# Kernel tuning notes

Measured on AMD Instinct MI355X. Metric: run time of the kernel, lower is better.

## Reference

```python
import jax, jax.numpy as jnp
import numpy as np

B, N, T_TOK, FEAT, H = 32, 64, 512, 768, 256


def setup_inputs() -> dict:
    key = jax.random.key(0)
    ks = jax.random.split(key, 16)
    p = lambda k, s: jax.random.normal(k, s, jnp.float32) * 0.02
    return {
        "hidden_state": jax.random.normal(ks[0], (B, T_TOK, FEAT), jnp.float32),
        "W_red": p(ks[1], (FEAT, H)), "b_red": jnp.zeros((H,), jnp.float32),
        "W_cat": p(ks[2], (2 * H, H)), "b_cat": jnp.zeros((H,), jnp.float32),
        "W_x": p(ks[3], (H, 3 * H)), "Us_zr": p(ks[4], (H, 2 * H)),
        "Us_h": p(ks[5], (H, H)), "b_g": jnp.zeros((3 * H,), jnp.float32),
        "W_e": p(ks[6], (H, 2)), "b_e": jnp.zeros((2,), jnp.float32),
        "W_c": p(ks[7], (H, 2)), "b_c": jnp.zeros((2,), jnp.float32),
        "W_t": p(ks[8], (H, 2)), "b_t": jnp.zeros((2,), jnp.float32),
        "bert_clause_b": jnp.sort(jax.random.randint(ks[9], (B, N), 0, T_TOK), axis=1),
        "y_mask_b": jnp.ones((B, N), jnp.int32),
    }


def _mdrnn(X, mask2d, W_x, Us_zr, Us_h, b_g):
    # Masked 2D GRU scanning the [B,N,N,H] doc matrix from top-left.
    Bh, Nn, Hd = X.shape[0], X.shape[1], Us_h.shape[0]
    xg = X @ W_x + b_g                       # precomputed input gates [B,N,N,3H]
    mf = mask2d.astype(X.dtype)[..., None]   # [B,N,N,1]

    def col_step(s_left, cols):
        xg_ij, s_up, m_ij = cols             # [B,3H], [B,H], [B,1]
        s_prev = 0.5 * (s_left + s_up)       # fuse left + up states
        zr = jax.nn.sigmoid(xg_ij[:, :2 * Hd] + s_prev @ Us_zr)
        z, r = zr[:, :Hd], zr[:, Hd:]
        h = jnp.tanh(xg_ij[:, 2 * Hd:] + (r * s_prev) @ Us_h)
        s = ((1.0 - z) * s_prev + z * h) * m_ij
        return s, s

    def row_step(prev_row, ins):
        xg_row, m_row = ins                  # [N,B,3H], [N,B,1]
        init = jnp.zeros((Bh, Hd), X.dtype)
        _, row = jax.lax.scan(col_step, init, (xg_row, jnp.swapaxes(prev_row, 0, 1), m_row))
        row = jnp.swapaxes(row, 0, 1)        # [B,N,H]
        return row, row

    xg_t = jnp.transpose(xg, (1, 2, 0, 3))   # [N(i), N(j), B, 3H]
    mf_t = jnp.transpose(mf, (1, 2, 0, 3))
    init_row = jnp.zeros((Bh, Nn, Hd), X.dtype)
    _, rows = jax.lax.scan(row_step, init_row, (xg_t, mf_t))
    return jnp.transpose(rows, (1, 0, 2, 3))  # [B,N,N,H]


def reference(hidden_state, W_red, b_red, W_cat, b_cat, W_x, Us_zr, Us_h, b_g,
              W_e, b_e, W_c, b_c, W_t, b_t, bert_clause_b, y_mask_b):
    # batched_index_select: gather clause-start token states
    doc = jnp.take_along_axis(hidden_state, bert_clause_b[..., None], axis=1)  # [B,N,FEAT]
    r = doc @ W_red + b_red                                                    # [B,N,H]
    Bh, Nn, Hd = r.shape
    # CatReduce: pairwise concat(r_i, r_j) -> Linear; then ReLU
    xi = jnp.broadcast_to(r[:, :, None, :], (Bh, Nn, Nn, Hd))
    xj = jnp.broadcast_to(r[:, None, :, :], (Bh, Nn, Nn, Hd))
    X = jax.nn.relu(jnp.concatenate([xi, xj], axis=-1) @ W_cat + b_cat)        # [B,N,N,H]
    mask2d = y_mask_b[:, None, :] & y_mask_b[:, :, None]                       # [B,N,N]
    Tm = _mdrnn(X, mask2d, W_x, Us_zr, Us_h, b_g)                              # [B,N,N,H]
    diag = jnp.transpose(jnp.diagonal(Tm, axis1=1, axis2=2), (0, 2, 1))        # [B,N,H]
    pred_e = diag @ W_e + b_e
    pred_c = diag @ W_c + b_c
    couples_pred = Tm @ W_t + b_t
    return couples_pred, pred_e, pred_c
```

## Files before the change

kernel.cpp:

```cpp
#include <hip/hip_runtime.h>
#include <hip/hip_bf16.h>

typedef float f32x4 __attribute__((ext_vector_type(4)));
typedef __bf16 bf16x8 __attribute__((ext_vector_type(8)));

using as1c_t = __attribute__((address_space(1))) const char;
using as3_t  = __attribute__((address_space(3))) char;

static __device__ __forceinline__ float sigmoidf_(float x) {
  return 1.f / (1.f + __expf(-x));
}
static __device__ __forceinline__ __bf16 bfc(float x) { return (__bf16)x; }

__global__ __launch_bounds__(256) void k_r(const float* __restrict__ hidden,
    const float* __restrict__ Wred, const float* __restrict__ bred,
    const int* __restrict__ cidx, float* __restrict__ r) {
  __shared__ float docsT[768][8];
  const int bx = blockIdx.x;
  const int b = bx >> 3, n0 = (bx & 7) * 8;
  const int t = threadIdx.x;
  #pragma unroll
  for (int g = 0; g < 8; ++g) {
    const int tok = cidx[b * 64 + n0 + g];
    const float* src = hidden + ((size_t)b * 512 + tok) * 768;
    for (int f = t; f < 768; f += 256) docsT[f][g] = src[f];
  }
  __syncthreads();
  float acc[8];
  #pragma unroll
  for (int g = 0; g < 8; ++g) acc[g] = bred[t];
  for (int f = 0; f < 768; ++f) {
    const float w = Wred[f * 256 + t];
    const float4 d0 = *(const float4*)&docsT[f][0];
    const float4 d1 = *(const float4*)&docsT[f][4];
    acc[0] = fmaf(d0.x, w, acc[0]); acc[1] = fmaf(d0.y, w, acc[1]);
    acc[2] = fmaf(d0.z, w, acc[2]); acc[3] = fmaf(d0.w, w, acc[3]);
    acc[4] = fmaf(d1.x, w, acc[4]); acc[5] = fmaf(d1.y, w, acc[5]);
    acc[6] = fmaf(d1.z, w, acc[6]); acc[7] = fmaf(d1.w, w, acc[7]);
  }
  #pragma unroll
  for (int g = 0; g < 8; ++g) r[((size_t)(b * 64 + n0 + g)) * 256 + t] = acc[g];
}

__global__ __launch_bounds__(256) void k_ab(const float* __restrict__ r,
    const float* __restrict__ Wcat, const float* __restrict__ bcat,
    float* __restrict__ Ai, float* __restrict__ Aj) {
  __shared__ float rT[256][8];
  const int bx = blockIdx.x;
  const int b = bx >> 3, n0 = (bx & 7) * 8;
  const int t = threadIdx.x;
  #pragma unroll
  for (int g = 0; g < 8; ++g)
    rT[t][g] = r[((size_t)(b * 64 + n0 + g)) * 256 + t];
  __syncthreads();
  float ai[8], aj[8];
  #pragma unroll
  for (int g = 0; g < 8; ++g) { ai[g] = bcat[t]; aj[g] = 0.f; }
  for (int k = 0; k < 256; ++k) {
    const float w0 = Wcat[k * 256 + t];
    const float w1 = Wcat[(256 + k) * 256 + t];
    const float4 d0 = *(const float4*)&rT[k][0];
    const float4 d1 = *(const float4*)&rT[k][4];
    ai[0] = fmaf(d0.x, w0, ai[0]); aj[0] = fmaf(d0.x, w1, aj[0]);
    ai[1] = fmaf(d0.y, w0, ai[1]); aj[1] = fmaf(d0.y, w1, aj[1]);
    ai[2] = fmaf(d0.z, w0, ai[2]); aj[2] = fmaf(d0.z, w1, aj[2]);
    ai[3] = fmaf(d0.w, w0, ai[3]); aj[3] = fmaf(d0.w, w1, aj[3]);
    ai[4] = fmaf(d1.x, w0, ai[4]); aj[4] = fmaf(d1.x, w1, aj[4]);
    ai[5] = fmaf(d1.y, w0, ai[5]); aj[5] = fmaf(d1.y, w1, aj[5]);
    ai[6] = fmaf(d1.z, w0, ai[6]); aj[6] = fmaf(d1.z, w1, aj[6]);
    ai[7] = fmaf(d1.w, w0, ai[7]); aj[7] = fmaf(d1.w, w1, aj[7]);
  }
  #pragma unroll
  for (int g = 0; g < 8; ++g) {
    Ai[((size_t)(b * 64 + n0 + g)) * 256 + t] = ai[g];
    Aj[((size_t)(b * 64 + n0 + g)) * 256 + t] = aj[g];
  }
}

__global__ __launch_bounds__(256) void k_wt(const float* __restrict__ Wx,
                                            __hip_bfloat16* __restrict__ WxT) {
  const int n = blockIdx.x, k = threadIdx.x;
  WxT[n * 256 + k] = __float2bfloat16(Wx[k * 768 + n]);
}

__global__ __launch_bounds__(256) void k_gemm(const float* __restrict__ Ai,
    const float* __restrict__ Aj, const __hip_bfloat16* __restrict__ WxT,
    const float* __restrict__ bg, __hip_bfloat16* __restrict__ xg,
    const int b_off) {
  __shared__ alignas(128) char smem[32768];
  char* const smA = smem;
  char* const smB = smem + 16384;
  const int t = threadIdx.x;
  const int lane = t & 63, w = t >> 6;
  const int wr = w >> 1, wc = w & 1;
  const int m0 = blockIdx.x * 128;
  const int n0 = blockIdx.y * 128;
  const char* const Wb = (const char*)WxT;

  const int b = b_off + (m0 >> 12);
  const int ibase = (m0 >> 6) & 63;
  const int rr = t >> 1, half = t & 1;
  const int jj_ = rr & 63, ii_ = ibase + (rr >> 6);
  const float* const aiRow = Ai + ((size_t)b * 64 + ii_) * 256 + half * 32;
  const float* const ajRow = Aj + ((size_t)b * 64 + jj_) * 256 + half * 32;
  char* const dstA = smA + rr * 128 + half * 64;

  f32x4 acc[4][4];
  const f32x4 zero = {0.f, 0.f, 0.f, 0.f};
  #pragma unroll
  for (int a2 = 0; a2 < 4; ++a2)
    #pragma unroll
    for (int b2 = 0; b2 < 4; ++b2) acc[a2][b2] = zero;

  for (int s = 0; s < 4; ++s) {
    const int k0 = s * 64;
    #pragma unroll
    for (int q = 0; q < 4; ++q) {
      const float4 a0 = *(const float4*)(aiRow + k0 + q * 8);
      const float4 a1 = *(const float4*)(aiRow + k0 + q * 8 + 4);
      const float4 c0 = *(const float4*)(ajRow + k0 + q * 8);
      const float4 c1 = *(const float4*)(ajRow + k0 + q * 8 + 4);
      bf16x8 v;
      v[0] = bfc(fmaxf(a0.x + c0.x, 0.f)); v[1] = bfc(fmaxf(a0.y + c0.y, 0.f));
      v[2] = bfc(fmaxf(a0.z + c0.z, 0.f)); v[3] = bfc(fmaxf(a0.w + c0.w, 0.f));
      v[4] = bfc(fmaxf(a1.x + c1.x, 0.f)); v[5] = bfc(fmaxf(a1.y + c1.y, 0.f));
      v[6] = bfc(fmaxf(a1.z + c1.z, 0.f)); v[7] = bfc(fmaxf(a1.w + c1.w, 0.f));
      *(bf16x8*)(dstA + q * 16) = v;
    }
    #pragma unroll
    for (int q = 0; q < 4; ++q) {
      const int chunk = w * 4 + q;
      const int tt2 = chunk * 1024 + lane * 16;
      const int row = tt2 >> 7;
      const int kb = tt2 & 0x7f;
      __builtin_amdgcn_global_load_lds(
          (as1c_t*)(Wb + (size_t)(n0 + row) * 512 + s * 128 + kb),
          (as3_t*)(smB + chunk * 1024), 16, 0, 0);
    }
    __syncthreads();
    #pragma unroll
    for (int kk = 0; kk < 2; ++kk) {
      bf16x8 af[4], bfr[4];
      const int kloc = kk * 64 + ((lane >> 4) << 4);
      #pragma unroll
      for (int ft = 0; ft < 4; ++ft) {
        const int rowa = wr * 64 + ft * 16 + (lane & 15);
        af[ft] = *(const bf16x8*)(smA + rowa * 128 + kloc);
      }
      #pragma unroll
      for (int fn = 0; fn < 4; ++fn) {
        const int rowb = wc * 64 + fn * 16 + (lane & 15);
        bfr[fn] = *(const bf16x8*)(smB + rowb * 128 + kloc);
      }
      #pragma unroll
      for (int ft = 0; ft < 4; ++ft)
        #pragma unroll
        for (int fn = 0; fn < 4; ++fn)
          acc[ft][fn] = __builtin_amdgcn_mfma_f32_16x16x32_bf16(
              af[ft], bfr[fn], acc[ft][fn], 0, 0, 0);
    }
    __syncthreads();
  }

  #pragma unroll
  for (int ft = 0; ft < 4; ++ft) {
    const int mbase = m0 + wr * 64 + ft * 16 + ((lane >> 4) << 2);
    #pragma unroll
    for (int fn = 0; fn < 4; ++fn) {
      const int n = n0 + wc * 64 + fn * 16 + (lane & 15);
      const float bias = bg[n];
      #pragma unroll
      for (int jj = 0; jj < 4; ++jj)
        xg[(size_t)(mbase + jj) * 768 + n] = __float2bfloat16(acc[ft][fn][jj] + bias);
    }
  }
}

__global__ __launch_bounds__(256) void k_diag(const int d, const int ilo,
    const int b_off, const __hip_bfloat16* __restrict__ xg,
    const float* __restrict__ Uzr, const float* __restrict__ Ush,
    const float* __restrict__ Sr, float* __restrict__ Sw,
    const float* __restrict__ Wt, const float* __restrict__ bt,
    const int* __restrict__ ym,
    float* __restrict__ couples, float* __restrict__ diagbuf) {
  __shared__ float sp[256][8];
  __shared__ float rs[256][8];
  __shared__ float red[4][16];
  const int t = threadIdx.x;
  const int i = ilo + blockIdx.x;
  const int j = d - i;
  const int b0 = b_off + blockIdx.y * 8;

  #pragma unroll
  for (int bb = 0; bb < 8; ++bb) {
    const int b = b0 + bb;
    const size_t base = ((size_t)(b * 64 + i)) * 256 + t;
    const float sl = (j > 0) ? Sr[base] : 0.f;
    const float su = (i > 0) ? Sr[base - 256] : 0.f;
    sp[t][bb] = 0.5f * (sl + su);
  }
  __syncthreads();

  const int c = t;
  float accz[8], accr[8];
  #pragma unroll
  for (int bb = 0; bb < 8; ++bb) {
    const size_t xrow = ((size_t)(b0 + bb - b_off) * 4096 + (size_t)i * 64 + j) * 768;
    accz[bb] = __bfloat162float(xg[xrow + c]);
    accr[bb] = __bfloat162float(xg[xrow + 256 + c]);
  }
  for (int k = 0; k < 256; ++k) {
    const float w0 = Uzr[k * 512 + c];
    const float w1 = Uzr[k * 512 + 256 + c];
    const float4 s0 = *(const float4*)&sp[k][0];
    const float4 s1 = *(const float4*)&sp[k][4];
    accz[0] = fmaf(s0.x, w0, accz[0]); accr[0] = fmaf(s0.x, w1, accr[0]);
    accz[1] = fmaf(s0.y, w0, accz[1]); accr[1] = fmaf(s0.y, w1, accr[1]);
    accz[2] = fmaf(s0.z, w0, accz[2]); accr[2] = fmaf(s0.z, w1, accr[2]);
    accz[3] = fmaf(s0.w, w0, accz[3]); accr[3] = fmaf(s0.w, w1, accr[3]);
    accz[4] = fmaf(s1.x, w0, accz[4]); accr[4] = fmaf(s1.x, w1, accr[4]);
    accz[5] = fmaf(s1.y, w0, accz[5]); accr[5] = fmaf(s1.y, w1, accr[5]);
    accz[6] = fmaf(s1.z, w0, accz[6]); accr[6] = fmaf(s1.z, w1, accr[6]);
    accz[7] = fmaf(s1.w, w0, accz[7]); accr[7] = fmaf(s1.w, w1, accr[7]);
  }
  float zv[8];
  #pragma unroll
  for (int bb = 0; bb < 8; ++bb) {
    zv[bb] = sigmoidf_(accz[bb]);
    const float rr = sigmoidf_(accr[bb]);
    rs[c][bb] = rr * sp[c][bb];
  }
  __syncthreads();

  float acch[8];
  #pragma unroll
  for (int bb = 0; bb < 8; ++bb) {
    const size_t xrow = ((size_t)(b0 + bb - b_off) * 4096 + (size_t)i * 64 + j) * 768;
    acch[bb] = __bfloat162float(xg[xrow + 512 + c]);
  }
  for (int k = 0; k < 256; ++k) {
    const float w = Ush[k * 256 + c];
    const float4 r0 = *(const float4*)&rs[k][0];
    const float4 r1 = *(const float4*)&rs[k][4];
    acch[0] = fmaf(r0.x, w, acch[0]); acch[1] = fmaf(r0.y, w, acch[1]);
    acch[2] = fmaf(r0.z, w, acch[2]); acch[3] = fmaf(r0.w, w, acch[3]);
    acch[4] = fmaf(r1.x, w, acch[4]); acch[5] = fmaf(r1.y, w, acch[5]);
    acch[6] = fmaf(r1.z, w, acch[6]); acch[7] = fmaf(r1.w, w, acch[7]);
  }
  float cp[16];
  #pragma unroll
  for (int bb = 0; bb < 8; ++bb) {
    const int b = b0 + bb;
    const float h = tanhf(acch[bb]);
    const float spv = sp[c][bb];
    float sv = (1.f - zv[bb]) * spv + zv[bb] * h;
    sv *= (float)(ym[b * 64 + i] & ym[b * 64 + j]);
    Sw[((size_t)(b * 64 + i)) * 256 + c] = sv;
    if (i == j) diagbuf[((size_t)(b * 64 + i)) * 256 + c] = sv;
    cp[bb * 2 + 0] = sv * Wt[c * 2 + 0];
    cp[bb * 2 + 1] = sv * Wt[c * 2 + 1];
  }
  #pragma unroll
  for (int v = 0; v < 16; ++v) {
    float x = cp[v];
    x += __shfl_xor(x, 1);  x += __shfl_xor(x, 2);  x += __shfl_xor(x, 4);
    x += __shfl_xor(x, 8);  x += __shfl_xor(x, 16); x += __shfl_xor(x, 32);
    cp[v] = x;
  }
  if ((t & 63) == 0) {
    #pragma unroll
    for (int v = 0; v < 16; ++v) red[t >> 6][v] = cp[v];
  }
  __syncthreads();
  if (t < 16) {
    const float x = red[0][t] + red[1][t] + red[2][t] + red[3][t];
    const int bb = t >> 1, o = t & 1;
    couples[(((size_t)(b0 + bb) * 4096) + (size_t)i * 64 + j) * 2 + o] = x + bt[o];
  }
}

__global__ __launch_bounds__(256) void k_head(const float* __restrict__ diagbuf,
    const float* __restrict__ We, const float* __restrict__ be,
    const float* __restrict__ Wc, const float* __restrict__ bc,
    float* __restrict__ pe, float* __restrict__ pc) {
  __shared__ float red[4][4];
  const int bn = blockIdx.x;
  const int t = threadIdx.x;
  const float s = diagbuf[(size_t)bn * 256 + t];
  float v[4] = { s * We[t * 2], s * We[t * 2 + 1], s * Wc[t * 2], s * Wc[t * 2 + 1] };
  #pragma unroll
  for (int q = 0; q < 4; ++q) {
    float x = v[q];
    x += __shfl_xor(x, 1);  x += __shfl_xor(x, 2);  x += __shfl_xor(x, 4);
    x += __shfl_xor(x, 8);  x += __shfl_xor(x, 16); x += __shfl_xor(x, 32);
    v[q] = x;
  }
  if ((t & 63) == 0) {
    #pragma unroll
    for (int q = 0; q < 4; ++q) red[t >> 6][q] = v[q];
  }
  __syncthreads();
  if (t < 4) {
    const float x = red[0][t] + red[1][t] + red[2][t] + red[3][t];
    if (t < 2) pe[bn * 2 + t] = x + be[t];
    else       pc[bn * 2 + (t - 2)] = x + bc[t - 2];
  }
}

extern "C" void kernel_launch(void* const* d_in, const int* in_sizes, int n_in,
                              void* d_out, int out_size, void* d_ws, size_t ws_size,
                              hipStream_t stream) {
  const float* hidden = (const float*)d_in[0];
  const float* Wred = (const float*)d_in[1];
  const float* bred = (const float*)d_in[2];
  const float* Wcat = (const float*)d_in[3];
  const float* bcat = (const float*)d_in[4];
  const float* Wx   = (const float*)d_in[5];
  const float* Uzr  = (const float*)d_in[6];
  const float* Ush  = (const float*)d_in[7];
  const float* bg   = (const float*)d_in[8];
  const float* We   = (const float*)d_in[9];
  const float* be   = (const float*)d_in[10];
  const float* Wc   = (const float*)d_in[11];
  const float* bc   = (const float*)d_in[12];
  const float* Wt   = (const float*)d_in[13];
  const float* bt   = (const float*)d_in[14];
  const int* cidx   = (const int*)d_in[15];
  const int* ym     = (const int*)d_in[16];

  char* ws = (char*)d_ws;
  const size_t MB2 = 2097152;
  float* r    = (float*)(ws);
  float* Ai   = (float*)(ws + 1 * MB2);
  float* Aj   = (float*)(ws + 2 * MB2);
  float* diag = (float*)(ws + 3 * MB2);
  float* S0   = (float*)(ws + 4 * MB2);
  float* S1   = (float*)(ws + 5 * MB2);
  __hip_bfloat16* WxT = (__hip_bfloat16*)(ws + 6 * MB2);
  const size_t xg_off = 6 * MB2 + 393216;
  __hip_bfloat16* xg  = (__hip_bfloat16*)(ws + xg_off);

  const size_t XG_FULL = (size_t)131072 * 768 * 2;
  int g = 4;
  if (ws_size >= xg_off + XG_FULL) g = 1;
  else if (ws_size >= xg_off + XG_FULL / 2) g = 2;
  const int Bg = 32 / g;
  const int Mg = Bg * 4096;

  float* couples = (float*)d_out;
  float* pe = couples + 262144;
  float* pc = couples + 266240;

  k_r<<<256, 256, 0, stream>>>(hidden, Wred, bred, cidx, r);
  k_ab<<<256, 256, 0, stream>>>(r, Wcat, bcat, Ai, Aj);
  k_wt<<<768, 256, 0, stream>>>(Wx, WxT);

  for (int grp = 0; grp < g; ++grp) {
    const int b_off = grp * Bg;
    k_gemm<<<dim3(Mg / 128, 6), 256, 0, stream>>>(Ai, Aj, WxT, bg, xg, b_off);
    for (int d = 0; d < 127; ++d) {
      const int ilo = d > 63 ? d - 63 : 0;
      const int ihi = d < 63 ? d : 63;
      const int L = ihi - ilo + 1;
      const float* Srd = (d & 1) ? S0 : S1;
      float* Swr = (d & 1) ? S1 : S0;
      k_diag<<<dim3(L, Bg / 8), 256, 0, stream>>>(d, ilo, b_off, xg, Uzr, Ush,
                                                  Srd, Swr, Wt, bt, ym,
                                                  couples, diag);
    }
  }
  k_head<<<2048, 256, 0, stream>>>(diag, We, be, Wc, bc, pe, pc);
}
```

Before: 3.702 ms.

## Replace per-diagonal launches with persistent wavefront kernel using flag-based row handoff

Replaces the 127 per-anti-diagonal kernel launches (possibly repeated per batch group) with one persistent kernel of 256 blocks, one per (row, batch-group). Each block walks its row's columns and receives the upper state from the previous row's block through a double-buffered ring in global memory, using producer/consumer atomic flags with spin-waits. This removes launch overhead and the global state ping-pong, and keeps the left state in registers. It assumes all 256 blocks are co-resident (otherwise deadlock) and drops the workspace-size fallback by always computing the full xg in one GEMM launch.

```diff
diff --git a/kernel.cpp b/kernel.cpp
--- a/kernel.cpp
+++ b/kernel.cpp
@@ -85,8 +85,7 @@
 
 __global__ __launch_bounds__(256) void k_gemm(const float* __restrict__ Ai,
     const float* __restrict__ Aj, const __hip_bfloat16* __restrict__ WxT,
-    const float* __restrict__ bg, __hip_bfloat16* __restrict__ xg,
-    const int b_off) {
+    const float* __restrict__ bg, __hip_bfloat16* __restrict__ xg) {
   __shared__ alignas(128) char smem[32768];
   char* const smA = smem;
   char* const smB = smem + 16384;
@@ -97,7 +96,7 @@
   const int n0 = blockIdx.y * 128;
   const char* const Wb = (const char*)WxT;
 
-  const int b = b_off + (m0 >> 12);
+  const int b = m0 >> 12;
   const int ibase = (m0 >> 6) & 63;
   const int rr = t >> 1, half = t & 1;
   const int jj_ = rr & 63, ii_ = ibase + (rr >> 6);
@@ -176,106 +175,145 @@
   }
 }
 
-__global__ __launch_bounds__(256) void k_diag(const int d, const int ilo,
-    const int b_off, const __hip_bfloat16* __restrict__ xg,
+__global__ __launch_bounds__(256) void k_wave(const __hip_bfloat16* __restrict__ xg,
     const float* __restrict__ Uzr, const float* __restrict__ Ush,
-    const float* __restrict__ Sr, float* __restrict__ Sw,
     const float* __restrict__ Wt, const float* __restrict__ bt,
     const int* __restrict__ ym,
-    float* __restrict__ couples, float* __restrict__ diagbuf) {
+    float* __restrict__ couples, float* __restrict__ diagbuf,
+    float* __restrict__ ring, int* __restrict__ prod, int* __restrict__ cons) {
   __shared__ float sp[256][8];
   __shared__ float rs[256][8];
   __shared__ float red[4][16];
   const int t = threadIdx.x;
-  const int i = ilo + blockIdx.x;
-  const int j = d - i;
-  const int b0 = b_off + blockIdx.y * 8;
-
-  #pragma unroll
-  for (int bb = 0; bb < 8; ++bb) {
-    const int b = b0 + bb;
-    const size_t base = ((size_t)(b * 64 + i)) * 256 + t;
-    const float sl = (j > 0) ? Sr[base] : 0.f;
-    const float su = (i > 0) ? Sr[base - 256] : 0.f;
-    sp[t][bb] = 0.5f * (sl + su);
-  }
-  __syncthreads();
-
   const int c = t;
-  float accz[8], accr[8];
-  #pragma unroll
-  for (int bb = 0; bb < 8; ++bb) {
-    const size_t xrow = ((size_t)(b0 + bb - b_off) * 4096 + (size_t)i * 64 + j) * 768;
-    accz[bb] = __bfloat162float(xg[xrow + c]);
-    accr[bb] = __bfloat162float(xg[xrow + 256 + c]);
-  }
-  for (int k = 0; k < 256; ++k) {
-    const float w0 = Uzr[k * 512 + c];
-    const float w1 = Uzr[k * 512 + 256 + c];
-    const float4 s0 = *(const float4*)&sp[k][0];
-    const float4 s1 = *(const float4*)&sp[k][4];
-    accz[0] = fmaf(s0.x, w0, accz[0]); accr[0] = fmaf(s0.x, w1, accr[0]);
-    accz[1] = fmaf(s0.y, w0, accz[1]); accr[1] = fmaf(s0.y, w1, accr[1]);
-    accz[2] = fmaf(s0.z, w0, accz[2]); accr[2] = fmaf(s0.z, w1, accr[2]);
-    accz[3] = fmaf(s0.w, w0, accz[3]); accr[3] = fmaf(s0.w, w1, accr[3]);
-    accz[4] = fmaf(s1.x, w0, accz[4]); accr[4] = fmaf(s1.x, w1, accr[4]);
-    accz[5] = fmaf(s1.y, w0, accz[5]); accr[5] = fmaf(s1.y, w1, accr[5]);
-    accz[6] = fmaf(s1.z, w0, accz[6]); accr[6] = fmaf(s1.z, w1, accr[6]);
-    accz[7] = fmaf(s1.w, w0, accz[7]); accr[7] = fmaf(s1.w, w1, accr[7]);
-  }
-  float zv[8];
-  #pragma unroll
-  for (int bb = 0; bb < 8; ++bb) {
-    zv[bb] = sigmoidf_(accz[bb]);
-    const float rr = sigmoidf_(accr[bb]);
-    rs[c][bb] = rr * sp[c][bb];
-  }
-  __syncthreads();
-
-  float acch[8];
-  #pragma unroll
-  for (int bb = 0; bb < 8; ++bb) {
-    const size_t xrow = ((size_t)(b0 + bb - b_off) * 4096 + (size_t)i * 64 + j) * 768;
-    acch[bb] = __bfloat162float(xg[xrow + 512 + c]);
-  }
-  for (int k = 0; k < 256; ++k) {
-    const float w = Ush[k * 256 + c];
-    const float4 r0 = *(const float4*)&rs[k][0];
-    const float4 r1 = *(const float4*)&rs[k][4];
-    acch[0] = fmaf(r0.x, w, acch[0]); acch[1] = fmaf(r0.y, w, acch[1]);
-    acch[2] = fmaf(r0.z, w, acch[2]); acch[3] = fmaf(r0.w, w, acch[3]);
-    acch[4] = fmaf(r1.x, w, acch[4]); acch[5] = fmaf(r1.y, w, acch[5]);
-    acch[6] = fmaf(r1.z, w, acch[6]); acch[7] = fmaf(r1.w, w, acch[7]);
-  }
-  float cp[16];
-  #pragma unroll
-  for (int bb = 0; bb < 8; ++bb) {
-    const int b = b0 + bb;
-    const float h = tanhf(acch[bb]);
-    const float spv = sp[c][bb];
-    float sv = (1.f - zv[bb]) * spv + zv[bb] * h;
-    sv *= (float)(ym[b * 64 + i] & ym[b * 64 + j]);
-    Sw[((size_t)(b * 64 + i)) * 256 + c] = sv;
-    if (i == j) diagbuf[((size_t)(b * 64 + i)) * 256 + c] = sv;
-    cp[bb * 2 + 0] = sv * Wt[c * 2 + 0];
-    cp[bb * 2 + 1] = sv * Wt[c * 2 + 1];
-  }
-  #pragma unroll
-  for (int v = 0; v < 16; ++v) {
-    float x = cp[v];
-    x += __shfl_xor(x, 1);  x += __shfl_xor(x, 2);  x += __shfl_xor(x, 4);
-    x += __shfl_xor(x, 8);  x += __shfl_xor(x, 16); x += __shfl_xor(x, 32);
-    cp[v] = x;
-  }
-  if ((t & 63) == 0) {
-    #pragma unroll
-    for (int v = 0; v < 16; ++v) red[t >> 6][v] = cp[v];
-  }
-  __syncthreads();
-  if (t < 16) {
-    const float x = red[0][t] + red[1][t] + red[2][t] + red[3][t];
-    const int bb = t >> 1, o = t & 1;
-    couples[(((size_t)(b0 + bb) * 4096) + (size_t)i * 64 + j) * 2 + o] = x + bt[o];
+  const int bx = blockIdx.x;
+  const int i = bx >> 2, bg = bx & 3;
+  const int b0 = bg * 8;
+
+  int* const pprev = prod + ((i - 1) * 4 + bg);
+  int* const pcons_self = cons + (i * 4 + bg);
+  int* const pcons_next = cons + ((i + 1) * 4 + bg);
+  int* const pprod_self = prod + (i * 4 + bg);
+  const float* const ring_rd = ring + (size_t)((i - 1) * 4 + bg) * 2 * 2048;
+  float* const ring_wr = ring + (size_t)(i * 4 + bg) * 2 * 2048;
+
+  float sl[8];
+  #pragma unroll
+  for (int bb = 0; bb < 8; ++bb) sl[bb] = 0.f;
+  int mi[8];
+  #pragma unroll
+  for (int bb = 0; bb < 8; ++bb) mi[bb] = ym[(b0 + bb) * 64 + i];
+
+  for (int j = 0; j < 64; ++j) {
+    float su[8];
+    if (i > 0) {
+      while (__hip_atomic_load(pprev, __ATOMIC_RELAXED, __HIP_MEMORY_SCOPE_AGENT) < j + 1)
+        __builtin_amdgcn_s_sleep(2);
+      __threadfence();
+      const float* src = ring_rd + (j & 1) * 2048 + c * 8;
+      const float4 u0 = *(const float4*)(src);
+      const float4 u1 = *(const float4*)(src + 4);
+      su[0] = u0.x; su[1] = u0.y; su[2] = u0.z; su[3] = u0.w;
+      su[4] = u1.x; su[5] = u1.y; su[6] = u1.z; su[7] = u1.w;
+    } else {
+      #pragma unroll
+      for (int bb = 0; bb < 8; ++bb) su[bb] = 0.f;
+    }
+    #pragma unroll
+    for (int bb = 0; bb < 8; ++bb) sp[c][bb] = 0.5f * (sl[bb] + su[bb]);
+    __syncthreads();
+    if (i > 0 && t == 0)
+      __hip_atomic_store(pcons_self, j + 1, __ATOMIC_RELAXED, __HIP_MEMORY_SCOPE_AGENT);
+
+    float accz[8], accr[8];
+    #pragma unroll
+    for (int bb = 0; bb < 8; ++bb) {
+      const size_t xrow = ((size_t)(b0 + bb) * 4096 + (size_t)i * 64 + j) * 768;
+      accz[bb] = __bfloat162float(xg[xrow + c]);
+      accr[bb] = __bfloat162float(xg[xrow + 256 + c]);
+    }
+    for (int k = 0; k < 256; ++k) {
+      const float w0 = Uzr[k * 512 + c];
+      const float w1 = Uzr[k * 512 + 256 + c];
+      const float4 s0 = *(const float4*)&sp[k][0];
+      const float4 s1 = *(const float4*)&sp[k][4];
+      accz[0] = fmaf(s0.x, w0, accz[0]); accr[0] = fmaf(s0.x, w1, accr[0]);
+      accz[1] = fmaf(s0.y, w0, accz[1]); accr[1] = fmaf(s0.y, w1, accr[1]);
+      accz[2] = fmaf(s0.z, w0, accz[2]); accr[2] = fmaf(s0.z, w1, accr[2]);
+      accz[3] = fmaf(s0.w, w0, accz[3]); accr[3] = fmaf(s0.w, w1, accr[3]);
+      accz[4] = fmaf(s1.x, w0, accz[4]); accr[4] = fmaf(s1.x, w1, accr[4]);
+      accz[5] = fmaf(s1.y, w0, accz[5]); accr[5] = fmaf(s1.y, w1, accr[5]);
+      accz[6] = fmaf(s1.z, w0, accz[6]); accr[6] = fmaf(s1.z, w1, accr[6]);
+      accz[7] = fmaf(s1.w, w0, accz[7]); accr[7] = fmaf(s1.w, w1, accr[7]);
+    }
+    float zv[8];
+    #pragma unroll
+    for (int bb = 0; bb < 8; ++bb) {
+      zv[bb] = sigmoidf_(accz[bb]);
+      const float rr = sigmoidf_(accr[bb]);
+      rs[c][bb] = rr * sp[c][bb];
+    }
+    __syncthreads();
+
+    float acch[8];
+    #pragma unroll
+    for (int bb = 0; bb < 8; ++bb) {
+      const size_t xrow = ((size_t)(b0 + bb) * 4096 + (size_t)i * 64 + j) * 768;
+      acch[bb] = __bfloat162float(xg[xrow + 512 + c]);
+    }
+    for (int k = 0; k < 256; ++k) {
+      const float w = Ush[k * 256 + c];
+      const float4 r0 = *(const float4*)&rs[k][0];
+      const float4 r1 = *(const float4*)&rs[k][4];
+      acch[0] = fmaf(r0.x, w, acch[0]); acch[1] = fmaf(r0.y, w, acch[1]);
+      acch[2] = fmaf(r0.z, w, acch[2]); acch[3] = fmaf(r0.w, w, acch[3]);
+      acch[4] = fmaf(r1.x, w, acch[4]); acch[5] = fmaf(r1.y, w, acch[5]);
+      acch[6] = fmaf(r1.z, w, acch[6]); acch[7] = fmaf(r1.w, w, acch[7]);
+    }
+    float cp[16];
+    #pragma unroll
+    for (int bb = 0; bb < 8; ++bb) {
+      const float h = tanhf(acch[bb]);
+      const float spv = sp[c][bb];
+      float sv = (1.f - zv[bb]) * spv + zv[bb] * h;
+      sv *= (float)(mi[bb] & ym[(b0 + bb) * 64 + j]);
+      sl[bb] = sv;
+      if (i == j) diagbuf[((size_t)((b0 + bb) * 64 + i)) * 256 + c] = sv;
+      cp[bb * 2 + 0] = sv * Wt[c * 2 + 0];
+      cp[bb * 2 + 1] = sv * Wt[c * 2 + 1];
+    }
+
+    if (i < 63) {
+      while (__hip_atomic_load(pcons_next, __ATOMIC_RELAXED, __HIP_MEMORY_SCOPE_AGENT) < j - 1)
+        __builtin_amdgcn_s_sleep(2);
+      float* dst = ring_wr + (j & 1) * 2048 + c * 8;
+      float4 v0, v1;
+      v0.x = sl[0]; v0.y = sl[1]; v0.z = sl[2]; v0.w = sl[3];
+      v1.x = sl[4]; v1.y = sl[5]; v1.z = sl[6]; v1.w = sl[7];
+      *(float4*)(dst) = v0;
+      *(float4*)(dst + 4) = v1;
+    }
+
+    #pragma unroll
+    for (int v = 0; v < 16; ++v) {
+      float x = cp[v];
+      x += __shfl_xor(x, 1);  x += __shfl_xor(x, 2);  x += __shfl_xor(x, 4);
+      x += __shfl_xor(x, 8);  x += __shfl_xor(x, 16); x += __shfl_xor(x, 32);
+      cp[v] = x;
+    }
+    if ((t & 63) == 0) {
+      #pragma unroll
+      for (int v = 0; v < 16; ++v) red[t >> 6][v] = cp[v];
+    }
+    __threadfence();
+    __syncthreads();
+    if (i < 63 && t == 0)
+      __hip_atomic_store(pprod_self, j + 1, __ATOMIC_RELAXED, __HIP_MEMORY_SCOPE_AGENT);
+    if (t < 16) {
+      const float x = red[0][t] + red[1][t] + red[2][t] + red[3][t];
+      const int bb = t >> 1, o = t & 1;
+      couples[(((size_t)(b0 + bb) * 4096) + (size_t)i * 64 + j) * 2 + o] = x + bt[o];
+    }
   }
 }
 
@@ -334,40 +372,25 @@
   float* Ai   = (float*)(ws + 1 * MB2);
   float* Aj   = (float*)(ws + 2 * MB2);
   float* diag = (float*)(ws + 3 * MB2);
-  float* S0   = (float*)(ws + 4 * MB2);
-  float* S1   = (float*)(ws + 5 * MB2);
-  __hip_bfloat16* WxT = (__hip_bfloat16*)(ws + 6 * MB2);
-  const size_t xg_off = 6 * MB2 + 393216;
-  __hip_bfloat16* xg  = (__hip_bfloat16*)(ws + xg_off);
-
-  const size_t XG_FULL = (size_t)131072 * 768 * 2;
-  int g = 4;
-  if (ws_size >= xg_off + XG_FULL) g = 1;
-  else if (ws_size >= xg_off + XG_FULL / 2) g = 2;
-  const int Bg = 32 / g;
-  const int Mg = Bg * 4096;
+  __hip_bfloat16* WxT = (__hip_bfloat16*)(ws + 4 * MB2);
+  char* flags = ws + 4 * MB2 + 393216;
+  int* prod = (int*)flags;
+  int* cons = (int*)(flags + 1024);
+  float* ring = (float*)(ws + 4 * MB2 + 393216 + 65536);
+  __hip_bfloat16* xg = (__hip_bfloat16*)(ws + 12976128 - 2 * MB2);
+  xg = (__hip_bfloat16*)(ws + (4 * MB2 + 393216 + 65536 + 4128768));
 
   float* couples = (float*)d_out;
   float* pe = couples + 262144;
   float* pc = couples + 266240;
 
+  hipMemsetAsync(flags, 0, 2048, stream);
+
   k_r<<<256, 256, 0, stream>>>(hidden, Wred, bred, cidx, r);
   k_ab<<<256, 256, 0, stream>>>(r, Wcat, bcat, Ai, Aj);
   k_wt<<<768, 256, 0, stream>>>(Wx, WxT);
-
-  for (int grp = 0; grp < g; ++grp) {
-    const int b_off = grp * Bg;
-    k_gemm<<<dim3(Mg / 128, 6), 256, 0, stream>>>(Ai, Aj, WxT, bg, xg, b_off);
-    for (int d = 0; d < 127; ++d) {
-      const int ilo = d > 63 ? d - 63 : 0;
-      const int ihi = d < 63 ? d : 63;
-      const int L = ihi - ilo + 1;
-      const float* Srd = (d & 1) ? S0 : S1;
-      float* Swr = (d & 1) ? S1 : S0;
-      k_diag<<<dim3(L, Bg / 8), 256, 0, stream>>>(d, ilo, b_off, xg, Uzr, Ush,
-                                                  Srd, Swr, Wt, bt, ym,
-                                                  couples, diag);
-    }
-  }
+  k_gemm<<<dim3(1024, 6), 256, 0, stream>>>(Ai, Aj, WxT, bg, xg);
+  k_wave<<<256, 256, 0, stream>>>(xg, Uzr, Ush, Wt, bt, ym,
+                                  couples, diag, ring, prod, cons);
   k_head<<<2048, 256, 0, stream>>>(diag, We, be, Wc, bc, pe, pc);
 }
```

New measurement: 8.268 ms. 2.23x slower.
